# Kernel tuning notes

Measured on AMD Instinct MI355X. Metric: run time of the kernel, lower is better.

The kernel has to match this reference:

```python
import jax, jax.numpy as jnp
import numpy as np

INPUT_NDIMS = 1024
HIDDEN = 512
LATENT = 50
BATCH = 16384

def setup_inputs() -> dict:
    key = jax.random.key(0)
    ks = jax.random.split(key, 12)
    s = 0.02
    x = jax.random.uniform(ks[0], (BATCH, INPUT_NDIMS), dtype=jnp.float32)
    u = 0.01 + 0.98 * jax.random.uniform(ks[1], (BATCH, LATENT), dtype=jnp.float32)
    W1 = s * jax.random.normal(ks[2], (HIDDEN, INPUT_NDIMS), dtype=jnp.float32)
    b1 = jnp.zeros((HIDDEN,), jnp.float32)
    Wa = s * jax.random.normal(ks[3], (LATENT, HIDDEN), dtype=jnp.float32)
    ba = jnp.zeros((LATENT,), jnp.float32)
    Wb = s * jax.random.normal(ks[4], (LATENT, HIDDEN), dtype=jnp.float32)
    bb = jnp.zeros((LATENT,), jnp.float32)
    W2 = s * jax.random.normal(ks[5], (HIDDEN, LATENT), dtype=jnp.float32)
    b2 = jnp.zeros((HIDDEN,), jnp.float32)
    W3 = s * jax.random.normal(ks[6], (INPUT_NDIMS, HIDDEN), dtype=jnp.float32)
    b3 = jnp.zeros((INPUT_NDIMS,), jnp.float32)
    return dict(x=x, u=u, W1=W1, b1=b1, Wa=Wa, ba=ba, Wb=Wb, bb=bb, W2=W2, b2=b2, W3=W3, b3=b3)

def _stick_segments(v):
    # pi[:, k] = v[:, k] * prod_{j<k} (1 - v[:, j])  -- single O(K) cumprod pass
    cp = jnp.cumprod(1.0 - v, axis=1)                       # inclusive cumprod
    excl = jnp.concatenate([jnp.ones_like(cp[:, :1]), cp[:, :-1]], axis=1)
    return v * excl

def reference(x, u, W1, b1, Wa, ba, Wb, bb, W2, b2, W3, b3):
    # encoder: MLP -> positive Kumaraswamy params alpha (param1), beta (param2)
    h = jax.nn.relu(x @ W1.T + b1)                           # [B, H]
    alpha = jax.nn.softplus(h @ Wa.T + ba) + 1e-4            # [B, K]
    beta = jax.nn.softplus(h @ Wb.T + bb) + 1e-4             # [B, K]
    # Kumaraswamy reparameterized sample: v = (1 - u^(1/beta))^(1/alpha)
    v = jnp.power(1.0 - jnp.power(u, 1.0 / beta), 1.0 / alpha)
    # set_v_K_to_one: force last stick fraction to 1 so segments sum to 1
    v = v.at[:, -1].set(1.0)
    pi = _stick_segments(v)                                  # [B, K], rows sum to 1
    # decoder: MLP with sigmoid output
    h2 = jax.nn.relu(pi @ W2.T + b2)                         # [B, H]
    recon = jax.nn.sigmoid(h2 @ W3.T + b3)                   # [B, D]
    return recon, alpha, beta
```

## Files before the change

kernel.cpp:

```cpp
#include <hip/hip_runtime.h>
#include <hip/hip_bf16.h>

typedef __hip_bfloat16 bf16_t;
typedef __attribute__((ext_vector_type(4))) float f32x4;
typedef __attribute__((ext_vector_type(8))) __bf16 bf16x8;
typedef __attribute__((ext_vector_type(8))) short s16x8;
typedef __attribute__((ext_vector_type(4))) unsigned short u16x4;

#define BATCH 16384
#define NDIM  1024
#define HID   512
#define LAT   50

#define LOG2E 1.44269504088896340736f
#define RLOG2E 0.69314718055994530942f

__device__ __forceinline__ float ex2(float x) { return __builtin_amdgcn_exp2f(x); }
__device__ __forceinline__ float lg2(float x) { return __builtin_amdgcn_logf(x); }
__device__ __forceinline__ float rcp(float x) { return __builtin_amdgcn_rcpf(x); }

__device__ inline unsigned short f2b_u(float f) {
  union { bf16_t b; unsigned short u; } cv; cv.b = __float2bfloat16(f); return cv.u;
}

__device__ __forceinline__ void gload16(const void* src, void* dst_lds) {
  __builtin_amdgcn_global_load_lds(
      reinterpret_cast<const __attribute__((address_space(1))) void*>(
          reinterpret_cast<unsigned long long>(src)),
      reinterpret_cast<__attribute__((address_space(3))) void*>(
          static_cast<unsigned>(reinterpret_cast<unsigned long long>(dst_lds))),
      16, 0, 0);
}

__global__ void prep_kernel(const float* __restrict__ x,  const float* __restrict__ W1,
                            const float* __restrict__ W3, const float* __restrict__ Wa,
                            const float* __restrict__ Wb, const float* __restrict__ W2,
                            const float* __restrict__ ba, const float* __restrict__ bb,
                            bf16_t* __restrict__ xb,  bf16_t* __restrict__ w1,
                            bf16_t* __restrict__ w3,  bf16_t* __restrict__ wab,
                            bf16_t* __restrict__ w2p, float* __restrict__ bab)
{
  const int XU   = (BATCH * NDIM) / 4;
  const int W1U  = (HID * NDIM) / 4;
  const int W3U  = (NDIM * HID) / 4;
  const int WABN = 128 * HID;
  const int W2PN = HID * 64;
  const int TOT  = XU + W1U + W3U + WABN + W2PN + 128;
  for (int i = blockIdx.x * blockDim.x + threadIdx.x; i < TOT;
       i += gridDim.x * blockDim.x) {
    int j = i;
    if (j < XU) {
      const f32x4 v = ((const f32x4*)x)[j];
      u16x4 o; o[0]=f2b_u(v[0]); o[1]=f2b_u(v[1]); o[2]=f2b_u(v[2]); o[3]=f2b_u(v[3]);
      ((u16x4*)xb)[j] = o; continue;
    }
    j -= XU;
    if (j < W1U) {
      const f32x4 v = ((const f32x4*)W1)[j];
      u16x4 o; o[0]=f2b_u(v[0]); o[1]=f2b_u(v[1]); o[2]=f2b_u(v[2]); o[3]=f2b_u(v[3]);
      ((u16x4*)w1)[j] = o; continue;
    }
    j -= W1U;
    if (j < W3U) {
      const f32x4 v = ((const f32x4*)W3)[j];
      u16x4 o; o[0]=f2b_u(v[0]); o[1]=f2b_u(v[1]); o[2]=f2b_u(v[2]); o[3]=f2b_u(v[3]);
      ((u16x4*)w3)[j] = o; continue;
    }
    j -= W3U;
    if (j < WABN) {
      const int n = j >> 9, k = j & 511;
      float v = (n < 50) ? Wa[n * 512 + k] : ((n < 100) ? Wb[(n - 50) * 512 + k] : 0.f);
      wab[j] = __float2bfloat16(v); continue;
    }
    j -= WABN;
    if (j < W2PN) {
      const int n = j >> 6, k = j & 63;
      w2p[j] = __float2bfloat16(k < 50 ? W2[n * 50 + k] : 0.f); continue;
    }
    j -= W2PN;
    bab[j] = (j < 50) ? ba[j] : ((j < 100) ? bb[j - 50] : 0.f);
  }
}

template<int EPI, int MT, int NT, int DB>
__global__ __launch_bounds__(512, 4)
void gemm_kernel(const bf16_t* __restrict__ A, const bf16_t* __restrict__ B,
                 const float* __restrict__ bias, void* __restrict__ out0,
                 int M, int N, int K)
{
  constexpr int MI  = MT / 32;
  constexpr int NI  = NT / 64;
  constexpr int IA  = MT / 64;
  constexpr int IB  = NT / 64;
  constexpr int BUF = MT * 128 + NT * 128;
  __shared__ char lds[(DB ? 2 : 1) * BUF];

  const int tid  = threadIdx.x;
  const int swzid = ((blockIdx.x & 7) * (gridDim.x >> 3)) + (blockIdx.x >> 3);
  const int nblocks = N / NT;
  const int bn   = swzid % nblocks;
  const int bm   = swzid / nblocks;
  const int wid  = tid >> 6;
  const int lane = tid & 63;
  const int l15  = lane & 15;
  const int l4   = lane >> 4;
  const int wm   = (wid >> 2) * (MT / 2);
  const int wn   = (wid & 3) * (NT / 4);
  const int uw   = __builtin_amdgcn_readfirstlane(wid);

  f32x4 acc[MI][NI] = {};

  auto stage_B = [&](char* buf, int k0) {
    char* lB = buf + MT * 128;
    #pragma unroll
    for (int i = 0; i < IB; ++i) {
      const int c  = (i * 8 + uw) * 64 + lane;
      const int r  = c >> 3;
      const int sp = c & 7;
      const int sl = sp ^ (r & 7);
      gload16(B + (size_t)(bn * NT + r) * K + k0 + sl * 8,
              lB + (i * 8 + uw) * 1024);
    }
  };
  auto stage_A = [&](char* buf, int k0) {
    #pragma unroll
    for (int i = 0; i < IA; ++i) {
      const int c  = (i * 8 + uw) * 64 + lane;
      const int r  = c >> 3;
      const int sp = c & 7;
      const int sl = sp ^ (r & 7);
      gload16(A + (size_t)(bm * MT + r) * K + k0 + sl * 8,
              buf + (i * 8 + uw) * 1024);
    }
  };
  auto compute = [&](const char* buf) {
    const char* lA = buf;
    const char* lB = buf + MT * 128;
    #pragma unroll
    for (int h = 0; h < 2; ++h) {
      bf16x8 af[MI], bfr[NI];
      #pragma unroll
      for (int mi = 0; mi < MI; ++mi) {
        const int row = wm + mi * 16 + l15;
        const int sp  = (h * 4 + l4) ^ (row & 7);
        af[mi] = *(const bf16x8*)(lA + row * 128 + sp * 16);
      }
      #pragma unroll
      for (int ni = 0; ni < NI; ++ni) {
        const int row = wn + ni * 16 + l15;
        const int sp  = (h * 4 + l4) ^ (row & 7);
        bfr[ni] = *(const bf16x8*)(lB + row * 128 + sp * 16);
      }
      #pragma unroll
      for (int mi = 0; mi < MI; ++mi)
        #pragma unroll
        for (int ni = 0; ni < NI; ++ni)
          acc[mi][ni] = __builtin_amdgcn_mfma_f32_16x16x32_bf16(
              af[mi], bfr[ni], acc[mi][ni], 0, 0, 0);
    }
  };

  const int nt = K >> 6;
  stage_A(lds, 0);
  stage_B(lds, 0);
  __syncthreads();

  int cur = 0;
  for (int t = 0; t < nt - 1; ++t) {
    char* nbuf = lds + (DB ? (cur ^ 1) * BUF : 0);
    const int k0n = (t + 1) << 6;
    stage_A(nbuf, k0n);
    stage_B(nbuf, k0n);
    compute(lds + cur * BUF);
    __syncthreads();
    cur ^= 1;
  }
  compute(lds + cur * BUF);

  #pragma unroll
  for (int ni = 0; ni < NI; ++ni) {
    const int n  = bn * NT + wn + ni * 16 + l15;
    const float bv = bias[n];
    #pragma unroll
    for (int mi = 0; mi < MI; ++mi) {
      #pragma unroll
      for (int r = 0; r < 4; ++r) {
        const int m  = bm * MT + wm + mi * 16 + l4 * 4 + r;
        const float t = acc[mi][ni][r] + bv;
        if (EPI == 0) {
          ((bf16_t*)out0)[(size_t)m * N + n] = __float2bfloat16(fmaxf(t, 0.f));
        } else {
          ((float*)out0)[(size_t)m * N + n] = rcp(1.f + ex2(-t * LOG2E));
        }
      }
    }
  }
}

__global__ __launch_bounds__(512, 2)
void abstick_kernel(const bf16_t* __restrict__ A, const bf16_t* __restrict__ wabg,
                    const float* __restrict__ bab, const bf16_t* __restrict__ w2pg,
                    const float* __restrict__ b2, const float* __restrict__ u,
                    float* __restrict__ out_a, float* __restrict__ out_b,
                    bf16_t* __restrict__ h2)
{
  constexpr int BUF = 64 * 128 + 16384;
  constexpr int PIL = 65536;
  constexpr int SMO = 73728;
  __shared__ char lds[100352];

  const int tid  = threadIdx.x;
  const int swzid = ((blockIdx.x & 7) * (gridDim.x >> 3)) + (blockIdx.x >> 3);
  const int bm   = swzid;
  const int wid  = tid >> 6;
  const int lane = tid & 63;
  const int l15  = lane & 15;
  const int l4   = lane >> 4;
  const int wm   = (wid >> 2) * 32;
  const int wn   = (wid & 3) * 32;
  const int uw   = __builtin_amdgcn_readfirstlane(wid);
  const int K    = HID;

  f32x4 acc[2][2] = {};

  auto stage_AB = [&](char* buf, int k0) {
    {
      const int c  = tid;
      const int r  = c >> 3;
      const int sp = c & 7;
      const int sl = sp ^ (r & 7);
      gload16(A + (size_t)(bm * 64 + r) * K + k0 + sl * 8, buf + uw * 1024);
    }
    char* lB = buf + 8192;
    #pragma unroll
    for (int i = 0; i < 2; ++i) {
      const int c  = (i * 8 + uw) * 64 + lane;
      const int r  = c >> 3;
      const int sp = c & 7;
      const int sl = sp ^ (r & 7);
      gload16(wabg + (size_t)r * K + k0 + sl * 8, lB + (i * 8 + uw) * 1024);
    }
  };
  auto compute1 = [&](const char* buf) {
    const char* lA = buf;
    const char* lB = buf + 8192;
    #pragma unroll
    for (int h = 0; h < 2; ++h) {
      bf16x8 af[2], bfr[2];
      #pragma unroll
      for (int mi = 0; mi < 2; ++mi) {
        const int row = wm + mi * 16 + l15;
        const int sp  = (h * 4 + l4) ^ (row & 7);
        af[mi] = *(const bf16x8*)(lA + row * 128 + sp * 16);
      }
      #pragma unroll
      for (int ni = 0; ni < 2; ++ni) {
        const int row = wn + ni * 16 + l15;
        const int sp  = (h * 4 + l4) ^ (row & 7);
        bfr[ni] = *(const bf16x8*)(lB + row * 128 + sp * 16);
      }
      #pragma unroll
      for (int mi = 0; mi < 2; ++mi)
        #pragma unroll
        for (int ni = 0; ni < 2; ++ni)
          acc[mi][ni] = __builtin_amdgcn_mfma_f32_16x16x32_bf16(
              af[mi], bfr[ni], acc[mi][ni], 0, 0, 0);
    }
  };

  stage_AB(lds, 0);
  __syncthreads();
  int cur = 0;
  for (int t = 0; t < 7; ++t) {
    stage_AB(lds + (cur ^ 1) * BUF, (t + 1) << 6);
    compute1(lds + cur * BUF);
    __syncthreads();
    cur ^= 1;
  }
  compute1(lds + cur * BUF);
  __syncthreads();

  #pragma unroll
  for (int i = 0; i < 8; ++i) {
    const int c  = (i * 8 + uw) * 64 + lane;
    const int r  = c >> 3;
    const int sp = c & 7;
    const int sl = sp ^ (r & 7);
    gload16(w2pg + (size_t)r * 64 + sl * 8, lds + (i * 8 + uw) * 1024);
  }

  float* sm = (float*)(lds + SMO);
  #pragma unroll
  for (int ni = 0; ni < 2; ++ni) {
    const int n  = wn + ni * 16 + l15;
    const float bv = bab[n];
    #pragma unroll
    for (int mi = 0; mi < 2; ++mi) {
      #pragma unroll
      for (int r = 0; r < 4; ++r) {
        const int ml = wm + mi * 16 + l4 * 4 + r;
        const int m  = bm * 64 + ml;
        const float t = acc[mi][ni][r] + bv;
        if (n < 100) {
          const float y =
              (t > 20.f ? t : lg2(1.f + ex2(t * LOG2E)) * RLOG2E) + 1e-4f;
          if (n < 50) out_a[(size_t)m * 50 + n] = y;
          else        out_b[(size_t)m * 50 + (n - 50)] = y;
          sm[ml * 104 + n + (n < 50 ? 0 : 2)] = y;
        }
      }
    }
  }
  __syncthreads();

  #pragma unroll 1
  for (int rr = 0; rr < 8; ++rr) {
    const int rl = wid * 8 + rr;
    const size_t m = (size_t)(bm * 64 + rl);
    float v = 1.f, t = 1.f;
    if (lane < 49) {
      const float a  = sm[rl * 104 + lane];
      const float b  = sm[rl * 104 + 52 + lane];
      const float uu = u[m * 50 + lane];
      const float tb = ex2(lg2(uu) * rcp(b));
      v = ex2(lg2(1.f - tb) * rcp(a));
      t = 1.f - v;
    }
    float p = t;
    #pragma unroll
    for (int d = 1; d < 64; d <<= 1) {
      const float o = __shfl_up(p, d, 64);
      if (lane >= d) p *= o;
    }
    float e = __shfl_up(p, 1, 64);
    if (lane == 0) e = 1.f;
    const float piv = (lane < 50) ? v * e : 0.f;
    *(unsigned short*)(lds + PIL + rl * 128 +
                       (((lane >> 3) ^ (rl & 7)) << 4) + ((lane & 7) << 1)) =
        f2b_u(piv);
  }
  __syncthreads();

  const int wn3 = (wid & 3) * 128;
  f32x4 acc3[2][8] = {};
  #pragma unroll
  for (int h = 0; h < 2; ++h) {
    bf16x8 af[2], bfr[8];
    #pragma unroll
    for (int mi = 0; mi < 2; ++mi) {
      const int row = wm + mi * 16 + l15;
      const int sp  = (h * 4 + l4) ^ (row & 7);
      af[mi] = *(const bf16x8*)(lds + PIL + row * 128 + sp * 16);
    }
    #pragma unroll
    for (int ni = 0; ni < 8; ++ni) {
      const int row = wn3 + ni * 16 + l15;
      const int sp  = (h * 4 + l4) ^ (row & 7);
      bfr[ni] = *(const bf16x8*)(lds + row * 128 + sp * 16);
    }
    #pragma unroll
    for (int mi = 0; mi < 2; ++mi)
      #pragma unroll
      for (int ni = 0; ni < 8; ++ni)
        acc3[mi][ni] = __builtin_amdgcn_mfma_f32_16x16x32_bf16(
            af[mi], bfr[ni], acc3[mi][ni], 0, 0, 0);
  }
  #pragma unroll
  for (int ni = 0; ni < 8; ++ni) {
    const int n  = wn3 + ni * 16 + l15;
    const float bv = b2[n];
    #pragma unroll
    for (int mi = 0; mi < 2; ++mi) {
      #pragma unroll
      for (int r = 0; r < 4; ++r) {
        const int m  = bm * 64 + wm + mi * 16 + l4 * 4 + r;
        h2[(size_t)m * HID + n] =
            __float2bfloat16(fmaxf(acc3[mi][ni][r] + bv, 0.f));
      }
    }
  }
}

extern "C" void kernel_launch(void* const* d_in, const int* in_sizes, int n_in,
                              void* d_out, int out_size, void* d_ws, size_t ws_size,
                              hipStream_t stream)
{
  const float* x  = (const float*)d_in[0];
  const float* u  = (const float*)d_in[1];
  const float* W1 = (const float*)d_in[2];
  const float* b1 = (const float*)d_in[3];
  const float* Wa = (const float*)d_in[4];
  const float* ba = (const float*)d_in[5];
  const float* Wb = (const float*)d_in[6];
  const float* bb = (const float*)d_in[7];
  const float* W2 = (const float*)d_in[8];
  const float* b2 = (const float*)d_in[9];
  const float* W3 = (const float*)d_in[10];
  const float* b3 = (const float*)d_in[11];

  float* recon  = (float*)d_out;
  float* oalpha = recon + (size_t)BATCH * NDIM;
  float* obeta  = oalpha + (size_t)BATCH * LAT;

  char* ws = (char*)d_ws;
  bf16_t* xb  = (bf16_t*)(ws);
  bf16_t* h2  = (bf16_t*)(ws);
  bf16_t* h   = (bf16_t*)(ws + 33554432);
  bf16_t* w1  = (bf16_t*)(ws + 50331648);
  bf16_t* w3  = (bf16_t*)(ws + 51380224);
  bf16_t* wab = (bf16_t*)(ws + 52428800);
  bf16_t* w2p = (bf16_t*)(ws + 52559872);
  float*  bab = (float*)(ws + 52625408);

  prep_kernel<<<2048, 256, 0, stream>>>(x, W1, W3, Wa, Wb, W2, ba, bb,
                                        xb, w1, w3, wab, w2p, bab);
  gemm_kernel<0, 64, 256, 1><<<512, 512, 0, stream>>>(
      xb, w1, b1, (void*)h, BATCH, HID, NDIM);
  abstick_kernel<<<256, 512, 0, stream>>>(
      h, wab, bab, w2p, b2, u, oalpha, obeta, h2);
  gemm_kernel<1, 64, 256, 1><<<1024, 512, 0, stream>>>(
      h2, w3, b3, (void*)recon, BATCH, NDIM, HID);
}
```

Measured before the change: 88.78 us.

## Prefetch two K-tiles ahead with explicit vmcnt waits in GEMM loops

Restructures the double-buffered K loops in the GEMM and abstick kernels so two tiles are in flight. Each iteration waits only for the older tile via s_waitcnt vmcnt, then computes, and then issues the load for tile t+2 into the freed buffer. This is meant to hide global-to-LDS latency behind MFMA work instead of draining all loads at every __syncthreads. It depends on the exact vmcnt count matching the number of loads per stage, and it adds a second barrier per iteration.

```diff
diff --git a/kernel.cpp b/kernel.cpp
--- a/kernel.cpp
+++ b/kernel.cpp
@@ -31,6 +31,12 @@
           static_cast<unsigned>(reinterpret_cast<unsigned long long>(dst_lds))),
       16, 0, 0);
 }
+
+#define WAIT_VMCNT(N)                                          \
+  do {                                                         \
+    asm volatile("s_waitcnt vmcnt(%0)" ::"i"(N) : "memory");   \
+    __builtin_amdgcn_sched_barrier(0);                         \
+  } while (0)
 
 __global__ void prep_kernel(const float* __restrict__ x,  const float* __restrict__ W1,
                             const float* __restrict__ W3, const float* __restrict__ Wa,
@@ -82,7 +88,7 @@
   }
 }
 
-template<int EPI, int MT, int NT, int DB>
+template<int EPI, int MT, int NT>
 __global__ __launch_bounds__(512, 4)
 void gemm_kernel(const bf16_t* __restrict__ A, const bf16_t* __restrict__ B,
                  const float* __restrict__ bias, void* __restrict__ out0,
@@ -92,8 +98,9 @@
   constexpr int NI  = NT / 64;
   constexpr int IA  = MT / 64;
   constexpr int IB  = NT / 64;
+  constexpr int L   = IA + IB;
   constexpr int BUF = MT * 128 + NT * 128;
-  __shared__ char lds[(DB ? 2 : 1) * BUF];
+  __shared__ char lds[2 * BUF];
 
   const int tid  = threadIdx.x;
   const int swzid = ((blockIdx.x & 7) * (gridDim.x >> 3)) + (blockIdx.x >> 3);
@@ -110,7 +117,16 @@
 
   f32x4 acc[MI][NI] = {};
 
-  auto stage_B = [&](char* buf, int k0) {
+  auto stage = [&](char* buf, int k0) {
+    #pragma unroll
+    for (int i = 0; i < IA; ++i) {
+      const int c  = (i * 8 + uw) * 64 + lane;
+      const int r  = c >> 3;
+      const int sp = c & 7;
+      const int sl = sp ^ (r & 7);
+      gload16(A + (size_t)(bm * MT + r) * K + k0 + sl * 8,
+              buf + (i * 8 + uw) * 1024);
+    }
     char* lB = buf + MT * 128;
     #pragma unroll
     for (int i = 0; i < IB; ++i) {
@@ -122,17 +138,6 @@
               lB + (i * 8 + uw) * 1024);
     }
   };
-  auto stage_A = [&](char* buf, int k0) {
-    #pragma unroll
-    for (int i = 0; i < IA; ++i) {
-      const int c  = (i * 8 + uw) * 64 + lane;
-      const int r  = c >> 3;
-      const int sp = c & 7;
-      const int sl = sp ^ (r & 7);
-      gload16(A + (size_t)(bm * MT + r) * K + k0 + sl * 8,
-              buf + (i * 8 + uw) * 1024);
-    }
-  };
   auto compute = [&](const char* buf) {
     const char* lA = buf;
     const char* lB = buf + MT * 128;
@@ -161,21 +166,17 @@
   };
 
   const int nt = K >> 6;
-  stage_A(lds, 0);
-  stage_B(lds, 0);
-  __syncthreads();
-
-  int cur = 0;
-  for (int t = 0; t < nt - 1; ++t) {
-    char* nbuf = lds + (DB ? (cur ^ 1) * BUF : 0);
-    const int k0n = (t + 1) << 6;
-    stage_A(nbuf, k0n);
-    stage_B(nbuf, k0n);
-    compute(lds + cur * BUF);
-    __syncthreads();
-    cur ^= 1;
-  }
-  compute(lds + cur * BUF);
+  stage(lds, 0);
+  if (nt > 1) stage(lds + BUF, 64);
+  for (int t = 0; t < nt; ++t) {
+    if (t + 1 < nt) WAIT_VMCNT(L);
+    else            WAIT_VMCNT(0);
+    __builtin_amdgcn_s_barrier();
+    compute(lds + (t & 1) * BUF);
+    __builtin_amdgcn_s_barrier();
+    __builtin_amdgcn_sched_barrier(0);
+    if (t + 2 < nt) stage(lds + (t & 1) * BUF, (t + 2) << 6);
+  }
 
   #pragma unroll
   for (int ni = 0; ni < NI; ++ni) {
@@ -269,16 +270,16 @@
   };
 
   stage_AB(lds, 0);
-  __syncthreads();
-  int cur = 0;
-  for (int t = 0; t < 7; ++t) {
-    stage_AB(lds + (cur ^ 1) * BUF, (t + 1) << 6);
-    compute1(lds + cur * BUF);
-    __syncthreads();
-    cur ^= 1;
-  }
-  compute1(lds + cur * BUF);
-  __syncthreads();
+  stage_AB(lds + BUF, 64);
+  for (int t = 0; t < 8; ++t) {
+    if (t + 1 < 8) WAIT_VMCNT(3);
+    else           WAIT_VMCNT(0);
+    __builtin_amdgcn_s_barrier();
+    compute1(lds + (t & 1) * BUF);
+    __builtin_amdgcn_s_barrier();
+    __builtin_amdgcn_sched_barrier(0);
+    if (t + 2 < 8) stage_AB(lds + (t & 1) * BUF, (t + 2) << 6);
+  }
 
   #pragma unroll
   for (int i = 0; i < 8; ++i) {
@@ -414,10 +415,10 @@
 
   prep_kernel<<<2048, 256, 0, stream>>>(x, W1, W3, Wa, Wb, W2, ba, bb,
                                         xb, w1, w3, wab, w2p, bab);
-  gemm_kernel<0, 64, 256, 1><<<512, 512, 0, stream>>>(
+  gemm_kernel<0, 64, 256><<<512, 512, 0, stream>>>(
       xb, w1, b1, (void*)h, BATCH, HID, NDIM);
   abstick_kernel<<<256, 512, 0, stream>>>(
       h, wab, bab, w2p, b2, u, oalpha, obeta, h2);
-  gemm_kernel<1, 64, 256, 1><<<1024, 512, 0, stream>>>(
+  gemm_kernel<1, 64, 256><<<1024, 512, 0, stream>>>(
       h2, w3, b3, (void*)recon, BATCH, NDIM, HID);
 }
```

After: 86.57 us. 2.5% less time.
